# Kernel tuning notes

Measured on AMD Instinct MI355X. Metric: run time of the kernel, lower is better.

## Reference

```python
import jax, jax.numpy as jnp
import numpy as np

B, N_IN, N = 8, 256, 8192
D, K = 64, 512


def setup_inputs() -> dict:
    key = jax.random.key(0)
    k1, k2, k3 = jax.random.split(key, 3)
    z = jax.random.normal(k1, (B, N_IN, N), dtype=jnp.float32)
    W = jax.random.normal(k2, (D, N_IN), dtype=jnp.float32) * (1.0 / np.sqrt(N_IN))
    emb = jax.random.normal(k3, (K, D), dtype=jnp.float32)
    ind_hist = jnp.zeros((K,), dtype=jnp.float32)
    return {"z": z, "W": W, "emb": emb, "ind_hist": ind_hist}


def reference(z, W, emb, ind_hist):
    # 1x1 Conv1d, no bias: (B, n_in, N) x (d, n_in) -> (B, d, N)
    ze = jnp.einsum('bin,di->bdn', z, W)
    emb_sg = jax.lax.stop_gradient(emb)  # StopGrad on codebook

    # Squared L2 distance ze[b,:,n] vs emb[k,:], expanded identity to avoid (B,K,d,N)
    ze_sq = jnp.sum(ze * ze, axis=1)                      # (B, N)
    emb_sq = jnp.sum(emb_sg * emb_sg, axis=1)             # (K,)
    cross = jnp.einsum('bdn,kd->bkn', ze, emb_sg)         # (B, K, N)
    l2norm_sq = ze_sq[:, None, :] + emb_sq[None, :, None] - 2.0 * cross  # (B, K, N)

    ind = jnp.argmin(l2norm_sq, axis=1)                   # (B, N) nearest code per timestep
    zq = jnp.take(emb_sg, ind, axis=0).transpose(0, 2, 1)  # (B, d, N)

    # ReplaceGrad straight-through: forward value zq, gradient routed to ze
    zq_rg = ze + jax.lax.stop_gradient(zq - ze)

    # Scatter histogram of chosen indices, accumulated into ind_hist buffer
    counts = jax.ops.segment_sum(
        jnp.ones((B * N,), dtype=ind_hist.dtype), ind.reshape(-1), num_segments=K)
    new_hist = ind_hist + counts

    return zq_rg, new_hist
```

## Files before the change

### kernel.cpp

```cpp
#include <hip/hip_runtime.h>

#define NIN    256
#define NCOL   8192
#define DDIM   64
#define KCODES 512
#define ZQ_ELEMS (8ull * 64ull * 8192ull)

__global__ __launch_bounds__(256) void vq_prep(const float* __restrict__ W,
                                               const float* __restrict__ emb,
                                               const float* __restrict__ ind_hist,
                                               float* __restrict__ Wt,
                                               float* __restrict__ embT,
                                               float* __restrict__ emb_sq,
                                               float* __restrict__ hist_out)
{
    const int t = blockIdx.x * 256 + threadIdx.x;
    if (t < NIN * DDIM) {
        int i = t >> 6;
        int d = t & 63;
        Wt[t] = W[d * NIN + i];
    }
    {
        int d = t >> 9;
        int k = t & 511;
        embT[t] = emb[k * DDIM + d];
    }
    if (t < KCODES) {
        const float* __restrict__ ek = emb + t * DDIM;
        float s = 0.f;
        #pragma unroll
        for (int d = 0; d < DDIM; ++d) s = fmaf(ek[d], ek[d], s);
        emb_sq[t] = s;
        hist_out[t] = ind_hist[t];
    }
}

__global__ __launch_bounds__(256, 4) void vq_main(const float* __restrict__ z,
                                                  const float* __restrict__ Wt,
                                                  const float* __restrict__ emb,
                                                  const float* __restrict__ embT,
                                                  const float* __restrict__ emb_sq,
                                                  float* __restrict__ out,
                                                  float* __restrict__ hist)
{
    __shared__ float ze_lds[64][DDIM + 1];
    __shared__ float bw_lds[4][64];
    __shared__ int   bk_lds[4][64];

    const int tid = threadIdx.x;
    const int cl  = tid & 63;
    const int w   = __builtin_amdgcn_readfirstlane(tid >> 6);
    const int C   = blockIdx.x * 64 + cl;
    const int b   = C >> 13;
    const int n   = C & (NCOL - 1);

    {
        const float* __restrict__ zp = z + (size_t)b * NIN * NCOL + n;
        const float* __restrict__ wp = Wt + w * 16;

        float acc[16];
        #pragma unroll
        for (int j = 0; j < 16; ++j) acc[j] = 0.f;

        for (int i = 0; i < NIN; i += 4) {
            float z0 = zp[(size_t)(i + 0) * NCOL];
            float z1 = zp[(size_t)(i + 1) * NCOL];
            float z2 = zp[(size_t)(i + 2) * NCOL];
            float z3 = zp[(size_t)(i + 3) * NCOL];
            const float* __restrict__ w0 = wp + (size_t)(i + 0) * DDIM;
            const float* __restrict__ w1 = wp + (size_t)(i + 1) * DDIM;
            const float* __restrict__ w2 = wp + (size_t)(i + 2) * DDIM;
            const float* __restrict__ w3 = wp + (size_t)(i + 3) * DDIM;
            #pragma unroll
            for (int j = 0; j < 16; ++j) {
                float a = acc[j];
                a = fmaf(w0[j], z0, a);
                a = fmaf(w1[j], z1, a);
                a = fmaf(w2[j], z2, a);
                a = fmaf(w3[j], z3, a);
                acc[j] = a;
            }
        }
        #pragma unroll
        for (int j = 0; j < 16; ++j) ze_lds[cl][w * 16 + j] = acc[j];
    }
    __syncthreads();

    float ze[DDIM];
    #pragma unroll
    for (int j = 0; j < DDIM; ++j) ze[j] = ze_lds[cl][j];

    float zesq = 0.f;
    #pragma unroll
    for (int d = 0; d < DDIM; ++d) zesq = fmaf(ze[d], ze[d], zesq);

    const int k0 = w * (KCODES / 4);
    float best  = 3.4e38f;
    int   bestk = k0;

    #pragma unroll 1
    for (int t8 = 0; t8 < 8; ++t8) {
        const int kt = k0 + t8 * 16;
        const float* __restrict__ ep0 = embT + kt;

        float acc[16];
        #pragma unroll
        for (int kk = 0; kk < 16; ++kk) acc[kk] = 0.f;

        #pragma unroll
        for (int j = 0; j < DDIM; ++j) {
            const float* __restrict__ ep = ep0 + (size_t)j * KCODES;
            const float zj = ze[j];
            #pragma unroll
            for (int kk = 0; kk < 16; ++kk)
                acc[kk] = fmaf(ep[kk], zj, acc[kk]);
        }

        #pragma unroll
        for (int kk = 0; kk < 16; ++kk) {
            const int k = kt + kk;
            float dist = (zesq + emb_sq[k]) - 2.0f * acc[kk];
            if (dist < best) { best = dist; bestk = k; }
        }
    }
    bw_lds[w][cl] = best;
    bk_lds[w][cl] = bestk;
    __syncthreads();

    float fb = bw_lds[0][cl];
    int   fk = bk_lds[0][cl];
    #pragma unroll
    for (int ww = 1; ww < 4; ++ww) {
        float v = bw_lds[ww][cl];
        int  kv = bk_lds[ww][cl];
        if (v < fb) { fb = v; fk = kv; }
    }

    if (w == 0) atomicAdd(hist + fk, 1.0f);

    const float4* __restrict__ eb =
        reinterpret_cast<const float4*>(emb + (size_t)fk * DDIM) + w * 4;
    float* __restrict__ op = out + ((size_t)b * DDIM + w * 16) * NCOL + n;
    #pragma unroll
    for (int v = 0; v < 4; ++v) {
        float4 e = eb[v];
        float z0 = ze_lds[cl][w * 16 + 4 * v + 0];
        float z1 = ze_lds[cl][w * 16 + 4 * v + 1];
        float z2 = ze_lds[cl][w * 16 + 4 * v + 2];
        float z3 = ze_lds[cl][w * 16 + 4 * v + 3];
        op[(size_t)(4 * v + 0) * NCOL] = z0 + (e.x - z0);
        op[(size_t)(4 * v + 1) * NCOL] = z1 + (e.y - z1);
        op[(size_t)(4 * v + 2) * NCOL] = z2 + (e.z - z2);
        op[(size_t)(4 * v + 3) * NCOL] = z3 + (e.w - z3);
    }
}

extern "C" void kernel_launch(void* const* d_in, const int* in_sizes, int n_in,
                              void* d_out, int out_size, void* d_ws, size_t ws_size,
                              hipStream_t stream)
{
    const float* z        = (const float*)d_in[0];
    const float* W        = (const float*)d_in[1];
    const float* emb      = (const float*)d_in[2];
    const float* ind_hist = (const float*)d_in[3];

    float* out  = (float*)d_out;
    float* hist = out + ZQ_ELEMS;

    float* Wt     = (float*)d_ws;
    float* embT   = Wt + NIN * DDIM;
    float* emb_sq = embT + DDIM * KCODES;

    hipLaunchKernelGGL(vq_prep, dim3(128), dim3(256), 0, stream,
                       W, emb, ind_hist, Wt, embT, emb_sq, hist);

    hipLaunchKernelGGL(vq_main, dim3(1024), dim3(256), 0, stream,
                       z, Wt, emb, embT, emb_sq, out, hist);
}
```

Before: 134.7 us.

## Split fused VQ kernel into separate conv and search kernels via output buffer

Splits the single fused kernel into a 1x1-conv kernel and a codebook-search kernel. The conv kernel uses 512-thread blocks with 8 outputs per wave, giving more waves to hide latency on the z stream. It writes ze into the output buffer, which the search kernel reads back and transposes into LDS. This trades an extra write and read of ze (about 16MB each way) plus one more launch for better occupancy in the memory-bound conv phase. It also pins the ze registers with asm volatile and makes the code offset wave-uniform via readfirstlane.

```diff
diff --git a/kernel.cpp b/kernel.cpp
--- a/kernel.cpp
+++ b/kernel.cpp
@@ -35,18 +35,10 @@
     }
 }
 
-__global__ __launch_bounds__(256, 4) void vq_main(const float* __restrict__ z,
+__global__ __launch_bounds__(512, 8) void vq_conv(const float* __restrict__ z,
                                                   const float* __restrict__ Wt,
-                                                  const float* __restrict__ emb,
-                                                  const float* __restrict__ embT,
-                                                  const float* __restrict__ emb_sq,
-                                                  float* __restrict__ out,
-                                                  float* __restrict__ hist)
-{
-    __shared__ float ze_lds[64][DDIM + 1];
-    __shared__ float bw_lds[4][64];
-    __shared__ int   bk_lds[4][64];
-
+                                                  float* __restrict__ out)
+{
     const int tid = threadIdx.x;
     const int cl  = tid & 63;
     const int w   = __builtin_amdgcn_readfirstlane(tid >> 6);
@@ -54,47 +46,85 @@
     const int b   = C >> 13;
     const int n   = C & (NCOL - 1);
 
+    const float* __restrict__ zp = z + (size_t)b * NIN * NCOL + n;
+    const float* __restrict__ wp = Wt + w * 8;
+
+    float acc[8];
+    #pragma unroll
+    for (int j = 0; j < 8; ++j) acc[j] = 0.f;
+
+    for (int i = 0; i < NIN; i += 4) {
+        float z0 = zp[(size_t)(i + 0) * NCOL];
+        float z1 = zp[(size_t)(i + 1) * NCOL];
+        float z2 = zp[(size_t)(i + 2) * NCOL];
+        float z3 = zp[(size_t)(i + 3) * NCOL];
+        const float* __restrict__ w0 = wp + (size_t)(i + 0) * DDIM;
+        const float* __restrict__ w1 = wp + (size_t)(i + 1) * DDIM;
+        const float* __restrict__ w2 = wp + (size_t)(i + 2) * DDIM;
+        const float* __restrict__ w3 = wp + (size_t)(i + 3) * DDIM;
+        #pragma unroll
+        for (int j = 0; j < 8; ++j) {
+            float a = acc[j];
+            a = fmaf(w0[j], z0, a);
+            a = fmaf(w1[j], z1, a);
+            a = fmaf(w2[j], z2, a);
+            a = fmaf(w3[j], z3, a);
+            acc[j] = a;
+        }
+    }
+
+    float* __restrict__ op = out + ((size_t)b * DDIM + w * 8) * NCOL + n;
+    #pragma unroll
+    for (int j = 0; j < 8; ++j) op[(size_t)j * NCOL] = acc[j];
+}
+
+__global__ __launch_bounds__(256, 4) void vq_searchfinal(
+        const float* __restrict__ zeb,
+        const float* __restrict__ emb,
+        const float* __restrict__ embT,
+        const float* __restrict__ emb_sq,
+        float* __restrict__ out,
+        float* __restrict__ hist)
+{
+    __shared__ float ze_lds[64][DDIM + 1];
+    __shared__ float bw_lds[4][64];
+    __shared__ int   bk_lds[4][64];
+
+    const int tid = threadIdx.x;
+    const int C0  = blockIdx.x * 64;
+    const int b   = C0 >> 13;
+    const int n0  = C0 & (NCOL - 1);
+
     {
-        const float* __restrict__ zp = z + (size_t)b * NIN * NCOL + n;
-        const float* __restrict__ wp = Wt + w * 16;
-
-        float acc[16];
-        #pragma unroll
-        for (int j = 0; j < 16; ++j) acc[j] = 0.f;
-
-        for (int i = 0; i < NIN; i += 4) {
-            float z0 = zp[(size_t)(i + 0) * NCOL];
-            float z1 = zp[(size_t)(i + 1) * NCOL];
-            float z2 = zp[(size_t)(i + 2) * NCOL];
-            float z3 = zp[(size_t)(i + 3) * NCOL];
-            const float* __restrict__ w0 = wp + (size_t)(i + 0) * DDIM;
-            const float* __restrict__ w1 = wp + (size_t)(i + 1) * DDIM;
-            const float* __restrict__ w2 = wp + (size_t)(i + 2) * DDIM;
-            const float* __restrict__ w3 = wp + (size_t)(i + 3) * DDIM;
-            #pragma unroll
-            for (int j = 0; j < 16; ++j) {
-                float a = acc[j];
-                a = fmaf(w0[j], z0, a);
-                a = fmaf(w1[j], z1, a);
-                a = fmaf(w2[j], z2, a);
-                a = fmaf(w3[j], z3, a);
-                acc[j] = a;
-            }
-        }
-        #pragma unroll
-        for (int j = 0; j < 16; ++j) ze_lds[cl][w * 16 + j] = acc[j];
+        const int r  = tid >> 2;
+        const int cc = (tid & 3) * 16;
+        const float4* __restrict__ src = reinterpret_cast<const float4*>(
+            zeb + ((size_t)b * DDIM + r) * NCOL + n0 + cc);
+        #pragma unroll
+        for (int v = 0; v < 4; ++v) {
+            float4 x = src[v];
+            ze_lds[cc + 4 * v + 0][r] = x.x;
+            ze_lds[cc + 4 * v + 1][r] = x.y;
+            ze_lds[cc + 4 * v + 2][r] = x.z;
+            ze_lds[cc + 4 * v + 3][r] = x.w;
+        }
     }
     __syncthreads();
 
+    const int cl = tid & 63;
+    const int w  = __builtin_amdgcn_readfirstlane(tid >> 6);
+
     float ze[DDIM];
     #pragma unroll
     for (int j = 0; j < DDIM; ++j) ze[j] = ze_lds[cl][j];
+    #pragma unroll
+    for (int j = 0; j < DDIM; ++j) asm volatile("" : "+v"(ze[j]));
 
     float zesq = 0.f;
     #pragma unroll
     for (int d = 0; d < DDIM; ++d) zesq = fmaf(ze[d], ze[d], zesq);
 
-    const int k0 = w * (KCODES / 4);
+    const int k0 = __builtin_amdgcn_readfirstlane(w * (KCODES / 4));
     float best  = 3.4e38f;
     int   bestk = k0;
 
@@ -138,6 +168,7 @@
 
     if (w == 0) atomicAdd(hist + fk, 1.0f);
 
+    const int n = n0 + cl;
     const float4* __restrict__ eb =
         reinterpret_cast<const float4*>(emb + (size_t)fk * DDIM) + w * 4;
     float* __restrict__ op = out + ((size_t)b * DDIM + w * 16) * NCOL + n;
@@ -174,6 +205,9 @@
     hipLaunchKernelGGL(vq_prep, dim3(128), dim3(256), 0, stream,
                        W, emb, ind_hist, Wt, embT, emb_sq, hist);
 
-    hipLaunchKernelGGL(vq_main, dim3(1024), dim3(256), 0, stream,
-                       z, Wt, emb, embT, emb_sq, out, hist);
-}
+    hipLaunchKernelGGL(vq_conv, dim3(1024), dim3(512), 0, stream,
+                       z, Wt, out);
+
+    hipLaunchKernelGGL(vq_searchfinal, dim3(1024), dim3(256), 0, stream,
+                       out, emb, embT, emb_sq, out, hist);
+}
```

Measured after the change: 142.0 us. +5.4%, slower.
